# Performance work log

Hardware: AMD Instinct MI355X
Metric: run time of the kernel (lower is better)

Reference implementation:

```python
import jax, jax.numpy as jnp
import numpy as np

B, C, T, NB, NF = 4, 256, 128, 64, 512

def _rms(x, w, eps=1e-6):
    # RMSNorm over channel dim (axis=1) of NCHW tensor
    return x * jax.lax.rsqrt(jnp.mean(x * x, axis=1, keepdims=True) + eps) * w[None, :, None, None]

def _conv1(x, w, b):
    # 1x1 conv: w is [out, in]
    return jnp.einsum('bchw,oc->bohw', x, w) + b[None, :, None, None]

def _swiglu(x, iw, ib, ow, ob):
    h = _conv1(x, iw, ib)
    a, g = jnp.split(h, 2, axis=1)
    return _conv1(a * jax.nn.silu(g), ow, ob)

def setup_inputs() -> dict:
    key = jax.random.key(0)
    ks = iter(jax.random.split(key, 32))
    s = lambda shape, scale: jax.random.normal(next(ks), shape, jnp.float32) * scale
    wsc = 1.0 / np.sqrt(C)
    return {
        'latent': s((B, C, T, NB), 1.0),
        'side': s((B, C, T, NF), 1.0),
        'expansion_basis': s((1, NB, 1, NF), 1.0),
        'lp_norm_w': jnp.ones((C,), jnp.float32),
        'lp_w': s((C, C), wsc), 'lp_b': jnp.zeros((C,), jnp.float32),
        'qn_w': jnp.ones((C,), jnp.float32),
        'qmlp_in_w': s((2 * C, C), wsc), 'qmlp_in_b': jnp.zeros((2 * C,), jnp.float32),
        'qmlp_out_w': s((C, C), wsc), 'qmlp_out_b': jnp.zeros((C,), jnp.float32),
        'q_w': s((C, C), wsc), 'q_b': jnp.zeros((C,), jnp.float32),
        'k_w': s((C, C), wsc), 'k_b': jnp.zeros((C,), jnp.float32),
        'v_w': s((C, C), wsc), 'v_b': jnp.zeros((C,), jnp.float32),
        'o_w': s((C, C), wsc), 'o_b': jnp.zeros((C,), jnp.float32),
        'ffn_norm_w': jnp.ones((C,), jnp.float32),
        'ffn_in_w': s((2 * C, C), wsc), 'ffn_in_b': jnp.zeros((2 * C,), jnp.float32),
        'ffn_out_w': s((C, C), wsc), 'ffn_out_b': jnp.zeros((C,), jnp.float32),
        'score_scale': jnp.asarray(1.0 / np.sqrt(C), jnp.float32),
        'prior_scale': jnp.asarray(1.0, jnp.float32),
        'query_skip_scale': jnp.asarray(1.0, jnp.float32),
    }

def reference(latent, side, expansion_basis, lp_norm_w, lp_w, lp_b, qn_w,
              qmlp_in_w, qmlp_in_b, qmlp_out_w, qmlp_out_b,
              q_w, q_b, k_w, k_b, v_w, v_b, o_w, o_b,
              ffn_norm_w, ffn_in_w, ffn_in_b, ffn_out_w, ffn_out_b,
              score_scale, prior_scale, query_skip_scale):
    # latent_pre: RMSNorm -> 1x1 conv -> SiLU
    latent_h = jax.nn.silu(_conv1(_rms(latent, lp_norm_w), lp_w, lp_b))  # [B,C,T,NB]
    # adaptive query path
    query_h = _swiglu(_rms(side, qn_w), qmlp_in_w, qmlp_in_b, qmlp_out_w, qmlp_out_b)  # [B,C,T,NF]
    q = _conv1(query_h, q_w, q_b)   # [B,C,T,NF]
    k = _conv1(latent_h, k_w, k_b)  # [B,C,T,NB]
    v = _conv1(latent_h, v_w, v_b)  # [B,C,T,NB]
    # scores: [B,T,NF,NB], contraction over channel
    scores = jnp.einsum('bctf,bctn->btfn', q, k) * score_scale
    bias = expansion_basis[0, :, 0, :].T  # [NF, NB]
    scores = scores + bias[None, None] * prior_scale
    weights = jax.nn.softmax(scores, axis=-1)
    attended = jnp.einsum('btfn,bctn->bctf', weights, v)  # [B,C,T,NF]
    hidden = _conv1(attended, o_w, o_b) + query_h * query_skip_scale
    hidden = hidden + _swiglu(_rms(hidden, ffn_norm_w), ffn_in_w, ffn_in_b, ffn_out_w, ffn_out_b)
    return hidden
```

## Files before the change

kernel.cpp:

```cpp
#include <hip/hip_runtime.h>
#include <stdint.h>
#include <stddef.h>

#define B_ 4
#define C_ 256
#define T_ 128
#define NB_ 64
#define NF_ 512
#define PLAT_ (T_*NB_)
#define PSIDE_ (T_*NF_)

using bf16x8 = __attribute__((ext_vector_type(8))) short;
using bf16x4 = __attribute__((ext_vector_type(4))) short;
using f32x4  = __attribute__((ext_vector_type(4))) float;

__device__ __forceinline__ float b2f(unsigned short h) {
  unsigned int u = ((unsigned int)h) << 16;
  return __builtin_bit_cast(float, u);
}
__device__ __forceinline__ unsigned short f2b(float f) {
  unsigned int u = __builtin_bit_cast(unsigned int, f);
  u += 0x7FFFu + ((u >> 16) & 1u);
  return (unsigned short)(u >> 16);
}

__device__ __forceinline__ bf16x8 ld8(const unsigned short* p) {
  return *(const bf16x8*)p;
}
__device__ __forceinline__ bf16x8 ld8(const float* p) {
  float4 a = *(const float4*)p;
  float4 b = *(const float4*)(p + 4);
  bf16x8 r;
  r[0] = (short)f2b(a.x); r[1] = (short)f2b(a.y);
  r[2] = (short)f2b(a.z); r[3] = (short)f2b(a.w);
  r[4] = (short)f2b(b.x); r[5] = (short)f2b(b.y);
  r[6] = (short)f2b(b.z); r[7] = (short)f2b(b.w);
  return r;
}
__device__ __forceinline__ float ldv(float v) { return v; }
__device__ __forceinline__ float ldv(unsigned short v) { return b2f(v); }
__device__ __forceinline__ void stv(float* p, float v) { *p = v; }
__device__ __forceinline__ void stv(unsigned short* p, float v) { *p = f2b(v); }

__device__ __forceinline__ void gload16(const void* g, void* l) {
  __builtin_amdgcn_global_load_lds(
      (const __attribute__((address_space(1))) void*)g,
      (__attribute__((address_space(3))) void*)l, 16, 0, 0);
}

__device__ __forceinline__ int u4i(int r) { return (r ^ (r >> 2)) & 3; }

enum { EPI_NONE = 0, EPI_SILU = 1, EPI_RESID = 3, EPI_SWIGLU = 4, EPI_DUALX = 5 };

__global__ __launch_bounds__(256) void wprep_k(const float* __restrict__ w,
                                               const float* __restrict__ nw,
                                               unsigned short* __restrict__ out, int n)
{
  int i = blockIdx.x * 256 + threadIdx.x;
  if (i < n) out[i] = f2b(w[i] * nw[i & 255]);
}

__global__ __launch_bounds__(256) void cvt_k(const float* __restrict__ in,
                                             unsigned short* __restrict__ out, int n)
{
  int i = blockIdx.x * 256 + threadIdx.x;
  if (i < n) out[i] = f2b(in[i]);
}

__global__ __launch_bounds__(256) void wscale_k(const float* __restrict__ w,
                                                const float* __restrict__ s,
                                                unsigned short* __restrict__ out, int n)
{
  int i = blockIdx.x * 256 + threadIdx.x;
  if (i < n) out[i] = f2b(w[i] * s[0]);
}

__global__ __launch_bounds__(256) void foldw_k(const float* __restrict__ A,
                                               const float* __restrict__ Bm,
                                               unsigned short* __restrict__ out)
{
  const int m = blockIdx.x;
  const int c = threadIdx.x;
  float acc = 0.f;
  #pragma unroll 8
  for (int j = 0; j < C_; ++j) acc = fmaf(A[m * C_ + j], Bm[j * C_ + c], acc);
  out[m * C_ + c] = f2b(acc);
}

__global__ __launch_bounds__(256) void foldb_k(const float* __restrict__ A,
                                               const float* __restrict__ bin,
                                               const float* __restrict__ badd,
                                               float* __restrict__ bout)
{
  const int m = threadIdx.x;
  float acc = 0.f;
  #pragma unroll 8
  for (int j = 0; j < C_; ++j) acc = fmaf(A[m * C_ + j], bin[j], acc);
  bout[m] = acc + badd[m];
}

__global__ __launch_bounds__(256) void bcomb_k(const float* __restrict__ b0,
                                               const float* __restrict__ b1,
                                               const float* __restrict__ s,
                                               float* __restrict__ bout)
{
  const int m = threadIdx.x;
  bout[m] = b0[m] + s[0] * b1[m];
}

template<int EPI, bool RMS, bool XT, typename TY, bool YT, int CFG>
__global__ __launch_bounds__(256, 2) void gemm_k(
    const void* __restrict__ Xv,
    const void* __restrict__ Xv2,
    const unsigned short* __restrict__ W,
    const float* __restrict__ bias,
    TY* Y,
    unsigned short* Y2,
    int Xs, int Xoff, int Ys, int Yoff, int Ys2)
{
  constexpr bool WDUAL = (EPI == EPI_SWIGLU) || (EPI == EPI_DUALX);
  constexpr bool GDUAL = (EPI == EPI_SWIGLU);
  constexpr bool XDUAL = (EPI == EPI_DUALX);
  constexpr bool H2    = (EPI == EPI_DUALX);
  constexpr int NWV = (CFG == 0) ? 1 : 2;
  constexpr int BM  = (CFG == 0) ? 256 : 128;
  constexpr int WN  = 64 / NWV;
  constexpr int NFR = WN / 16;
  constexpr int RW  = (WDUAL ? 2 : 1) * BM;
  constexpr int XR  = (XDUAL ? 2 : 1) * 64;

  __shared__ unsigned short sA[RW * 32];
  __shared__ unsigned short sX[XR * 32];
  __shared__ float red[4][64];

  const int tid = threadIdx.x;
  const int lane = tid & 63;
  const int wid = tid >> 6;
  const int l15 = lane & 15;
  const int q4 = lane >> 4;
  const int z = blockIdx.z;
  const int p0 = blockIdx.x * 64;
  const int m0 = blockIdx.y * BM;
  const int mh = (CFG == 0) ? wid : (wid >> 1);
  const int nh = (CFG == 0) ? 0 : (wid & 1);

  const float* Xf = nullptr;
  const unsigned short* Xt = nullptr;
  const unsigned short* Xt2 = nullptr;
  if constexpr (XT) {
    Xt = (const unsigned short*)Xv + ((size_t)z * Xs + Xoff + p0) * C_;
    if constexpr (XDUAL)
      Xt2 = (const unsigned short*)Xv2 + ((size_t)z * Xs + Xoff + p0) * C_;
  } else {
    Xf = (const float*)Xv + (size_t)z * C_ * Xs + Xoff + p0;
  }

  const f32x4 zf = {0.f, 0.f, 0.f, 0.f};
  f32x4 acc0[4][NFR];
  f32x4 acc1[GDUAL ? 4 : 1][NFR];
  #pragma unroll
  for (int i = 0; i < 4; ++i)
    #pragma unroll
    for (int j = 0; j < NFR; ++j) {
      acc0[i][j] = zf;
      if constexpr (GDUAL) acc1[i][j] = zf;
    }

  float sq = 0.f;

  for (int kt = 0; kt < 8; ++kt) {
    if constexpr (XT) {
      const int row = wid * 16 + (lane >> 2);
      const int chunk = (lane & 3) ^ u4i(row);
      const size_t soff = (size_t)row * C_ + kt * 32 + (chunk << 3);
      gload16(Xt + soff, &sX[(wid * 16) * 32]);
      if constexpr (XDUAL) gload16(Xt2 + soff, &sX[(64 + wid * 16) * 32]);
    } else {
      const float* xp = Xf + (size_t)(kt * 32 + wid * 8) * Xs + lane;
      float v[8];
      #pragma unroll
      for (int j = 0; j < 8; ++j) v[j] = xp[(size_t)j * Xs];
      bf16x8 w8;
      #pragma unroll
      for (int j = 0; j < 8; ++j) {
        if constexpr (RMS) sq = fmaf(v[j], v[j], sq);
        w8[j] = (short)f2b(v[j]);
      }
      *(bf16x8*)((char*)sX + lane * 64 + ((wid ^ u4i(lane)) << 4)) = w8;
    }
    #pragma unroll
    for (int it = 0; it < RW / 64; ++it) {
      const int rbase = wid * (RW / 4) + it * 16;
      const int rl = rbase + (lane >> 2);
      const int bank = rl / BM;
      const int rloc = rl & (BM - 1);
      const int chunk = (lane & 3) ^ u4i(rl);
      gload16(W + (size_t)(bank * C_ + m0 + rloc) * C_ + kt * 32 + (chunk << 3),
              &sA[rbase * 32]);
    }
    __syncthreads();

    bf16x8 af0[4], af1[4], bfr[NFR], bfr2[NFR];
    #pragma unroll
    for (int mf = 0; mf < 4; ++mf) {
      const int r = mh * 64 + mf * 16 + l15;
      const int sl = (q4 ^ u4i(r)) << 3;
      af0[mf] = *(const bf16x8*)(&sA[r * 32 + sl]);
      if constexpr (WDUAL) af1[mf] = *(const bf16x8*)(&sA[(BM + r) * 32 + sl]);
    }
    #pragma unroll
    for (int nf = 0; nf < NFR; ++nf) {
      const int n = nh * WN + nf * 16 + l15;
      const int sl = (q4 ^ u4i(n)) << 3;
      bfr[nf] = *(const bf16x8*)(&sX[n * 32 + sl]);
      if constexpr (XDUAL) bfr2[nf] = *(const bf16x8*)(&sX[(64 + n) * 32 + sl]);
    }
    #pragma unroll
    for (int mf = 0; mf < 4; ++mf)
      #pragma unroll
      for (int nf = 0; nf < NFR; ++nf) {
        acc0[mf][nf] = __builtin_amdgcn_mfma_f32_16x16x32_bf16(af0[mf], bfr[nf], acc0[mf][nf], 0, 0, 0);
        if constexpr (GDUAL)
          acc1[mf][nf] = __builtin_amdgcn_mfma_f32_16x16x32_bf16(af1[mf], bfr[nf], acc1[mf][nf], 0, 0, 0);
        if constexpr (XDUAL)
          acc0[mf][nf] = __builtin_amdgcn_mfma_f32_16x16x32_bf16(af1[mf], bfr2[nf], acc0[mf][nf], 0, 0, 0);
      }
    __syncthreads();
  }

  float cs[NFR];
  #pragma unroll
  for (int nf = 0; nf < NFR; ++nf) cs[nf] = 1.f;
  if constexpr (RMS) {
    red[wid][lane] = sq;
    __syncthreads();
    #pragma unroll
    for (int nf = 0; nf < NFR; ++nf) {
      const int n = nh * WN + nf * 16 + l15;
      cs[nf] = rsqrtf((red[0][n] + red[1][n] + red[2][n] + red[3][n]) * (1.0f / (float)C_) + 1e-6f);
    }
  }

  TY* Yb = nullptr;
  if constexpr (!YT) Yb = Y + (size_t)z * C_ * Ys + Yoff;

  float p2[NFR];
  #pragma unroll
  for (int nf = 0; nf < NFR; ++nf) p2[nf] = 0.f;

  #pragma unroll
  for (int mf = 0; mf < 4; ++mf) {
    const int mb = m0 + mh * 64 + mf * 16 + q4 * 4;
    const float4 b1 = *(const float4*)(bias + mb);
    float4 b2 = {0.f, 0.f, 0.f, 0.f};
    if constexpr (GDUAL) b2 = *(const float4*)(bias + C_ + mb);
    #pragma unroll
    for (int nf = 0; nf < NFR; ++nf) {
      const int pl = p0 + nh * WN + nf * 16 + l15;
      if constexpr (YT) {
        bf16x4 pk;
        #pragma unroll
        for (int r = 0; r < 4; ++r) {
          float y = acc0[mf][nf][r] * cs[nf] + ((const float*)&b1)[r];
          if constexpr (EPI == EPI_SILU) y = y / (1.0f + __expf(-y));
          if constexpr (EPI == EPI_SWIGLU) {
            float g = acc1[mf][nf][r] * cs[nf] + ((const float*)&b2)[r];
            y = y * (g / (1.0f + __expf(-g)));
          }
          pk[r] = (short)f2b(y);
        }
        *(bf16x4*)(Y + ((size_t)z * Ys + Yoff + pl) * C_ + mb) = pk;
      } else {
        #pragma unroll
        for (int r = 0; r < 4; ++r) {
          const size_t oidx = (size_t)(mb + r) * Ys + pl;
          float y = acc0[mf][nf][r] * cs[nf] + ((const float*)&b1)[r];
          if constexpr (EPI == EPI_SILU) y = y / (1.0f + __expf(-y));
          if constexpr (EPI == EPI_SWIGLU) {
            float g = acc1[mf][nf][r] * cs[nf] + ((const float*)&b2)[r];
            y = y * (g / (1.0f + __expf(-g)));
          }
          if constexpr (EPI == EPI_RESID) y += ldv(Yb[oidx]);
          if constexpr (H2) p2[nf] = fmaf(y, y, p2[nf]);
          stv(&Yb[oidx], y);
        }
      }
    }
  }

  if constexpr (H2) {
    #pragma unroll
    for (int nf = 0; nf < NFR; ++nf) {
      p2[nf] += __shfl_xor(p2[nf], 16);
      p2[nf] += __shfl_xor(p2[nf], 32);
    }
    if (q4 == 0) {
      #pragma unroll
      for (int nf = 0; nf < NFR; ++nf) red[wid][nf * 16 + l15] = p2[nf];
    }
    __syncthreads();
    float cs2[NFR];
    #pragma unroll
    for (int nf = 0; nf < NFR; ++nf) {
      const int n = nf * 16 + l15;
      cs2[nf] = rsqrtf((red[0][n] + red[1][n] + red[2][n] + red[3][n]) * (1.0f / (float)C_) + 1e-6f);
    }
    #pragma unroll
    for (int mf = 0; mf < 4; ++mf) {
      const int mb = m0 + mh * 64 + mf * 16 + q4 * 4;
      const float4 b1 = *(const float4*)(bias + mb);
      #pragma unroll
      for (int nf = 0; nf < NFR; ++nf) {
        const int pl = p0 + nf * 16 + l15;
        bf16x4 pk;
        #pragma unroll
        for (int r = 0; r < 4; ++r) {
          const float h = (acc0[mf][nf][r] + ((const float*)&b1)[r]) * cs2[nf];
          pk[r] = (short)f2b(h);
        }
        *(bf16x4*)(Y2 + ((size_t)z * Ys2 + pl) * C_ + mb) = pk;
      }
    }
  }
}

__global__ __launch_bounds__(256) void attn_k(
    const unsigned short* Q,
    const unsigned short* __restrict__ Kp,
    const unsigned short* __restrict__ Vp,
    const float* __restrict__ basis,
    const float* __restrict__ ssp,
    const float* __restrict__ psp,
    unsigned short* O,
    int PsQ, int t0, int ltc)
{
  __shared__ unsigned short sK[64 * 256];
  __shared__ unsigned short sQ[64 * 256];
  __shared__ unsigned short sV[256 * 72];
  __shared__ unsigned short sW[64 * 72];
  __shared__ unsigned short sB[64 * 72];

  const int tid = threadIdx.x;
  const int lane = tid & 63;
  const int wid = tid >> 6;
  const int l15 = lane & 15;
  const int q4 = lane >> 4;
  const int z = blockIdx.x >> ltc;
  const int tl = blockIdx.x & ((1 << ltc) - 1);

  const unsigned short* Qt = Q + ((size_t)z * PsQ + (size_t)tl * NF_) * C_;
  unsigned short*       Ot = O + ((size_t)z * PsQ + (size_t)tl * NF_) * C_;
  const unsigned short* Kt = Kp + ((size_t)z * PLAT_ + (size_t)(t0 + tl) * NB_) * C_;
  const size_t vbase = (size_t)z * C_ * PLAT_ + (size_t)(t0 + tl) * NB_;

  const float ss = ssp[0];
  const float ps = psp[0];
  const f32x4 zf = {0.f, 0.f, 0.f, 0.f};

  {
    #pragma unroll
    for (int it = 0; it < 8; ++it) {
      int i = wid * 8 + it;
      int n = 2 * i + (lane >> 5);
      int sc = (lane & 31) ^ (n & 7);
      gload16(Kt + (size_t)n * C_ + (sc << 3), &sK[i * 512]);
    }
    const int c0 = tid >> 3;
    const int n0 = (tid & 7) << 3;
    #pragma unroll
    for (int pass = 0; pass < 8; ++pass) {
      int c = c0 + pass * 32;
      bf16x8 v8 = *(const bf16x8*)(Vp + vbase + (size_t)c * PLAT_ + n0);
      *(bf16x8*)(&sV[c * 72 + n0]) = v8;
    }
  }

  for (int fc = 0; fc < 8; ++fc) {
    const int f0 = fc * 64;
    #pragma unroll
    for (int it = 0; it < 8; ++it) {
      int i = wid * 8 + it;
      int n = 2 * i + (lane >> 5);
      int sc = (lane & 31) ^ (n & 7);
      gload16(Qt + (size_t)(f0 + n) * C_ + (sc << 3), &sQ[i * 512]);
    }
    {
      const int nr = tid >> 3;
      const int fl0 = (tid & 7) << 3;
      #pragma unroll
      for (int pass = 0; pass < 2; ++pass) {
        int nn = nr + pass * 32;
        bf16x8 b8 = ld8(basis + (size_t)nn * NF_ + f0 + fl0);
        *(bf16x8*)(&sB[nn * 72 + fl0]) = b8;
      }
    }
    __syncthreads();

    f32x4 sacc[4];
    #pragma unroll
    for (int nt = 0; nt < 4; ++nt) sacc[nt] = zf;
    const int frow = wid * 16 + l15;
    const int swq = l15 & 7;
    #pragma unroll
    for (int kt = 0; kt < 8; ++kt) {
      int kb = kt * 4 + q4;
      bf16x8 a8 = *(const bf16x8*)(&sQ[frow * 256 + ((kb ^ swq) << 3)]);
      #pragma unroll
      for (int nt = 0; nt < 4; ++nt) {
        bf16x8 b8 = *(const bf16x8*)(&sK[(nt * 16 + l15) * 256 + ((kb ^ swq) << 3)]);
        sacc[nt] = __builtin_amdgcn_mfma_f32_16x16x32_bf16(a8, b8, sacc[nt], 0, 0, 0);
      }
    }

    #pragma unroll
    for (int r = 0; r < 4; ++r) {
      const int fcl = wid * 16 + q4 * 4 + r;
      float v[4];
      #pragma unroll
      for (int nt = 0; nt < 4; ++nt)
        v[nt] = sacc[nt][r] * ss + b2f(sB[(nt * 16 + l15) * 72 + fcl]) * ps;
      float mx = fmaxf(fmaxf(v[0], v[1]), fmaxf(v[2], v[3]));
      #pragma unroll
      for (int d = 1; d < 16; d <<= 1) mx = fmaxf(mx, __shfl_xor(mx, d));
      float e[4], sum = 0.f;
      #pragma unroll
      for (int nt = 0; nt < 4; ++nt) { e[nt] = __expf(v[nt] - mx); sum += e[nt]; }
      #pragma unroll
      for (int d = 1; d < 16; d <<= 1) sum += __shfl_xor(sum, d);
      float inv = 1.0f / sum;
      #pragma unroll
      for (int nt = 0; nt < 4; ++nt)
        sW[fcl * 72 + nt * 16 + l15] = f2b(e[nt] * inv);
    }
    __syncthreads();

    f32x4 pacc[4][4];
    #pragma unroll
    for (int mf = 0; mf < 4; ++mf)
      #pragma unroll
      for (int nf = 0; nf < 4; ++nf) pacc[mf][nf] = zf;
    #pragma unroll
    for (int kt = 0; kt < 2; ++kt) {
      int k0 = kt * 32 + q4 * 8;
      bf16x8 a8[4], b8[4];
      #pragma unroll
      for (int mf = 0; mf < 4; ++mf)
        a8[mf] = *(const bf16x8*)(&sV[(wid * 64 + mf * 16 + l15) * 72 + k0]);
      #pragma unroll
      for (int nf = 0; nf < 4; ++nf)
        b8[nf] = *(const bf16x8*)(&sW[(nf * 16 + l15) * 72 + k0]);
      #pragma unroll
      for (int mf = 0; mf < 4; ++mf)
        #pragma unroll
        for (int nf = 0; nf < 4; ++nf)
          pacc[mf][nf] = __builtin_amdgcn_mfma_f32_16x16x32_bf16(a8[mf], b8[nf], pacc[mf][nf], 0, 0, 0);
    }
    #pragma unroll
    for (int mf = 0; mf < 4; ++mf) {
      int cb = wid * 64 + mf * 16 + q4 * 4;
      #pragma unroll
      for (int nf = 0; nf < 4; ++nf) {
        int f = f0 + nf * 16 + l15;
        bf16x4 pk;
        #pragma unroll
        for (int r = 0; r < 4; ++r) pk[r] = (short)f2b(pacc[mf][nf][r]);
        *(bf16x4*)(Ot + (size_t)f * C_ + cb) = pk;
      }
    }
    __syncthreads();
  }
}

extern "C" void kernel_launch(void* const* d_in, const int* in_sizes, int n_in,
                              void* d_out, int out_size, void* d_ws, size_t ws_size,
                              hipStream_t stream)
{
  (void)in_sizes; (void)n_in; (void)out_size;
  const float* latent     = (const float*)d_in[0];
  const float* side       = (const float*)d_in[1];
  const float* basis      = (const float*)d_in[2];
  const float* lp_norm_w  = (const float*)d_in[3];
  const float* lp_w       = (const float*)d_in[4];
  const float* lp_b       = (const float*)d_in[5];
  const float* qn_w       = (const float*)d_in[6];
  const float* qmlp_in_w  = (const float*)d_in[7];
  const float* qmlp_in_b  = (const float*)d_in[8];
  const float* qmlp_out_w = (const float*)d_in[9];
  const float* qmlp_out_b = (const float*)d_in[10];
  const float* q_w        = (const float*)d_in[11];
  const float* q_b        = (const float*)d_in[12];
  const float* k_w        = (const float*)d_in[13];
  const float* k_b        = (const float*)d_in[14];
  const float* v_w        = (const float*)d_in[15];
  const float* v_b        = (const float*)d_in[16];
  const float* o_w        = (const float*)d_in[17];
  const float* o_b        = (const float*)d_in[18];
  const float* ffn_norm_w = (const float*)d_in[19];
  const float* ffn_in_w   = (const float*)d_in[20];
  const float* ffn_in_b   = (const float*)d_in[21];
  const float* ffn_out_w  = (const float*)d_in[22];
  const float* ffn_out_b  = (const float*)d_in[23];
  const float* sc_scale   = (const float*)d_in[24];
  const float* pr_scale   = (const float*)d_in[25];
  const float* qk_scale   = (const float*)d_in[26];
  float* out = (float*)d_out;

  auto align256 = [](size_t b) { return (b + 255) & ~(size_t)255; };
  const size_t fixed_bytes =
      5 * align256((size_t)C_ * C_ * 2) +
      3 * align256((size_t)2 * C_ * C_ * 2) +
      2 * align256((size_t)C_ * 4) +
      3 * align256((size_t)B_ * C_ * PLAT_ * 2);
  int nc = 16;
  for (int c = 1; c <= 16; c <<= 1) {
    size_t Pcb = (size_t)PSIDE_ / c;
    size_t need = fixed_bytes + 2 * align256((size_t)B_ * C_ * Pcb * 2);
    if (need <= ws_size) { nc = c; break; }
  }
  const int Pc  = PSIDE_ / nc;
  const int Tc  = T_ / nc;
  int ltc = 0; while ((1 << ltc) < Tc) ++ltc;

  char* ws = (char*)d_ws;
  size_t off = 0;
  auto carve = [&](size_t bytes) -> char* {
    char* p = ws + off;
    off += (bytes + 255) & ~(size_t)255;
    return p;
  };
  unsigned short* wlp      = (unsigned short*)carve((size_t)C_ * C_ * 2);
  unsigned short* wqin     = (unsigned short*)carve((size_t)2 * C_ * C_ * 2);
  unsigned short* wffin    = (unsigned short*)carve((size_t)2 * C_ * C_ * 2);
  unsigned short* wk       = (unsigned short*)carve((size_t)C_ * C_ * 2);
  unsigned short* wv       = (unsigned short*)carve((size_t)C_ * C_ * 2);
  unsigned short* wfo      = (unsigned short*)carve((size_t)C_ * C_ * 2);
  unsigned short* wqeff    = (unsigned short*)carve((size_t)C_ * C_ * 2);
  unsigned short* wocat    = (unsigned short*)carve((size_t)2 * C_ * C_ * 2);
  float*          beff     = (float*)carve((size_t)C_ * 4);
  float*          bcomb    = (float*)carve((size_t)C_ * 4);
  unsigned short* latent_h = (unsigned short*)carve((size_t)B_ * C_ * PLAT_ * 2);
  unsigned short* kbuf     = (unsigned short*)carve((size_t)B_ * C_ * PLAT_ * 2);
  unsigned short* vbuf     = (unsigned short*)carve((size_t)B_ * C_ * PLAT_ * 2);
  unsigned short* big0     = (unsigned short*)carve((size_t)B_ * C_ * Pc * 2);
  unsigned short* qbuf     = (unsigned short*)carve((size_t)B_ * C_ * Pc * 2);

  const dim3 blk(256);
  const dim3 gLatA(PLAT_ / 64, 1, B_);
  const dim3 gChA(Pc / 64, 1, B_);
  const dim3 gChB(Pc / 64, 2, B_);
  const int NW = C_ * C_;

  wprep_k<<<dim3(NW / 256), blk, 0, stream>>>(lp_w, lp_norm_w, wlp, NW);
  wprep_k<<<dim3(2 * NW / 256), blk, 0, stream>>>(qmlp_in_w, qn_w, wqin, 2 * NW);
  wprep_k<<<dim3(2 * NW / 256), blk, 0, stream>>>(ffn_in_w, ffn_norm_w, wffin, 2 * NW);
  cvt_k<<<dim3(NW / 256), blk, 0, stream>>>(k_w, wk, NW);
  cvt_k<<<dim3(NW / 256), blk, 0, stream>>>(v_w, wv, NW);
  cvt_k<<<dim3(NW / 256), blk, 0, stream>>>(ffn_out_w, wfo, NW);
  foldw_k<<<dim3(C_), blk, 0, stream>>>(q_w, qmlp_out_w, wqeff);
  foldb_k<<<dim3(1), blk, 0, stream>>>(q_w, qmlp_out_b, q_b, beff);
  cvt_k<<<dim3(NW / 256), blk, 0, stream>>>(o_w, wocat, NW);
  wscale_k<<<dim3(NW / 256), blk, 0, stream>>>(qmlp_out_w, qk_scale, wocat + (size_t)NW, NW);
  bcomb_k<<<dim3(1), blk, 0, stream>>>(o_b, qmlp_out_b, qk_scale, bcomb);

  gemm_k<EPI_SILU, true, false, unsigned short, true, 0><<<gLatA, blk, 0, stream>>>(
      latent, nullptr, wlp, lp_b, latent_h, nullptr, PLAT_, 0, PLAT_, 0, 0);
  gemm_k<EPI_NONE, false, true, unsigned short, true, 0><<<gLatA, blk, 0, stream>>>(
      latent_h, nullptr, wk, k_b, kbuf, nullptr, PLAT_, 0, PLAT_, 0, 0);
  gemm_k<EPI_NONE, false, true, unsigned short, false, 0><<<gLatA, blk, 0, stream>>>(
      latent_h, nullptr, wv, v_b, vbuf, nullptr, PLAT_, 0, PLAT_, 0, 0);

  for (int ch = 0; ch < nc; ++ch) {
    const int co = ch * Pc;
    const int t0 = ch * Tc;
    gemm_k<EPI_SWIGLU, true, false, unsigned short, true, 1><<<gChB, blk, 0, stream>>>(
        side, nullptr, wqin, qmlp_in_b, big0, nullptr, PSIDE_, co, Pc, 0, 0);
    gemm_k<EPI_NONE, false, true, unsigned short, true, 0><<<gChA, blk, 0, stream>>>(
        big0, nullptr, wqeff, beff, qbuf, nullptr, Pc, 0, Pc, 0, 0);
    attn_k<<<dim3(B_ * Tc), blk, 0, stream>>>(qbuf, kbuf, vbuf, basis, sc_scale, pr_scale,
                                              qbuf, Pc, t0, ltc);
    gemm_k<EPI_DUALX, false, true, float, false, 0><<<gChA, blk, 0, stream>>>(
        qbuf, big0, wocat, bcomb, out, qbuf, Pc, 0, PSIDE_, co, Pc);
    gemm_k<EPI_SWIGLU, false, true, unsigned short, true, 1><<<gChB, blk, 0, stream>>>(
        qbuf, nullptr, wffin, ffn_in_b, big0, nullptr, Pc, 0, Pc, 0, 0);
    gemm_k<EPI_RESID, false, true, float, false, 0><<<gChA, blk, 0, stream>>>(
        big0, nullptr, wfo, ffn_out_b, out, nullptr, Pc, 0, PSIDE_, co, 0);
  }
}
```

Baseline: 1.457 ms.

## Defer FFN RMS scaling to consumer GEMM and keep hidden in bf16

The DUALX GEMM no longer writes fp32 hidden to the output plus a normalized bf16 copy. It now writes unnormalized bf16 hidden into qbuf along with a per-position RMS scale vector. The FFN-in GEMM applies that scale in its epilogue (CSIN), and the final residual GEMM reads the bf16 hidden from qbuf instead of reading back fp32 output. This removes an fp32 write and read of the full output plus a second accumulator pass, at the cost of holding the residual in bf16 precision. The CFG1 grid is also flattened so the two M-halves of a pixel tile are adjacent block indices.

```diff
diff --git a/kernel.cpp b/kernel.cpp
--- a/kernel.cpp
+++ b/kernel.cpp
@@ -16,6 +16,10 @@
 
 __device__ __forceinline__ float b2f(unsigned short h) {
   unsigned int u = ((unsigned int)h) << 16;
+  return __builtin_bit_cast(float, u);
+}
+__device__ __forceinline__ float b2f(short h) {
+  unsigned int u = ((unsigned int)(unsigned short)h) << 16;
   return __builtin_bit_cast(float, u);
 }
 __device__ __forceinline__ unsigned short f2b(float f) {
@@ -37,8 +41,6 @@
   r[6] = (short)f2b(b.z); r[7] = (short)f2b(b.w);
   return r;
 }
-__device__ __forceinline__ float ldv(float v) { return v; }
-__device__ __forceinline__ float ldv(unsigned short v) { return b2f(v); }
 __device__ __forceinline__ void stv(float* p, float v) { *p = v; }
 __device__ __forceinline__ void stv(unsigned short* p, float v) { *p = f2b(v); }
 
@@ -108,22 +110,22 @@
   bout[m] = b0[m] + s[0] * b1[m];
 }
 
-template<int EPI, bool RMS, bool XT, typename TY, bool YT, int CFG>
+template<int EPI, bool RMS, bool XT, typename TY, bool YT, int CFG, bool CSIN>
 __global__ __launch_bounds__(256, 2) void gemm_k(
     const void* __restrict__ Xv,
     const void* __restrict__ Xv2,
     const unsigned short* __restrict__ W,
     const float* __restrict__ bias,
     TY* Y,
-    unsigned short* Y2,
-    int Xs, int Xoff, int Ys, int Yoff, int Ys2)
+    const unsigned short* __restrict__ RT,
+    float* pscale,
+    int Xs, int Xoff, int Ys, int Yoff, int Ps)
 {
   constexpr bool WDUAL = (EPI == EPI_SWIGLU) || (EPI == EPI_DUALX);
   constexpr bool GDUAL = (EPI == EPI_SWIGLU);
   constexpr bool XDUAL = (EPI == EPI_DUALX);
-  constexpr bool H2    = (EPI == EPI_DUALX);
+  constexpr int BM  = (CFG == 0) ? 256 : 128;
   constexpr int NWV = (CFG == 0) ? 1 : 2;
-  constexpr int BM  = (CFG == 0) ? 256 : 128;
   constexpr int WN  = 64 / NWV;
   constexpr int NFR = WN / 16;
   constexpr int RW  = (WDUAL ? 2 : 1) * BM;
@@ -139,8 +141,8 @@
   const int l15 = lane & 15;
   const int q4 = lane >> 4;
   const int z = blockIdx.z;
-  const int p0 = blockIdx.x * 64;
-  const int m0 = blockIdx.y * BM;
+  const int p0 = ((CFG == 0) ? blockIdx.x : (blockIdx.x >> 1)) * 64;
+  const int m0 = (CFG == 0) ? 0 : (blockIdx.x & 1) * BM;
   const int mh = (CFG == 0) ? wid : (wid >> 1);
   const int nh = (CFG == 0) ? 0 : (wid & 1);
 
@@ -240,6 +242,11 @@
       cs[nf] = rsqrtf((red[0][n] + red[1][n] + red[2][n] + red[3][n]) * (1.0f / (float)C_) + 1e-6f);
     }
   }
+  if constexpr (CSIN) {
+    #pragma unroll
+    for (int nf = 0; nf < NFR; ++nf)
+      cs[nf] = pscale[(size_t)z * Ps + p0 + nh * WN + nf * 16 + l15];
+  }
 
   TY* Yb = nullptr;
   if constexpr (!YT) Yb = Y + (size_t)z * C_ * Ys + Yoff;
@@ -257,6 +264,9 @@
     #pragma unroll
     for (int nf = 0; nf < NFR; ++nf) {
       const int pl = p0 + nh * WN + nf * 16 + l15;
+      bf16x4 h4 = {0, 0, 0, 0};
+      if constexpr (EPI == EPI_RESID)
+        h4 = *(const bf16x4*)(RT + ((size_t)z * Ps + pl) * C_ + mb);
       if constexpr (YT) {
         bf16x4 pk;
         #pragma unroll
@@ -267,6 +277,7 @@
             float g = acc1[mf][nf][r] * cs[nf] + ((const float*)&b2)[r];
             y = y * (g / (1.0f + __expf(-g)));
           }
+          if constexpr (EPI == EPI_DUALX) p2[nf] = fmaf(y, y, p2[nf]);
           pk[r] = (short)f2b(y);
         }
         *(bf16x4*)(Y + ((size_t)z * Ys + Yoff + pl) * C_ + mb) = pk;
@@ -280,15 +291,14 @@
             float g = acc1[mf][nf][r] * cs[nf] + ((const float*)&b2)[r];
             y = y * (g / (1.0f + __expf(-g)));
           }
-          if constexpr (EPI == EPI_RESID) y += ldv(Yb[oidx]);
-          if constexpr (H2) p2[nf] = fmaf(y, y, p2[nf]);
+          if constexpr (EPI == EPI_RESID) y += b2f(h4[r]);
           stv(&Yb[oidx], y);
         }
       }
     }
   }
 
-  if constexpr (H2) {
+  if constexpr (EPI == EPI_DUALX) {
     #pragma unroll
     for (int nf = 0; nf < NFR; ++nf) {
       p2[nf] += __shfl_xor(p2[nf], 16);
@@ -299,26 +309,12 @@
       for (int nf = 0; nf < NFR; ++nf) red[wid][nf * 16 + l15] = p2[nf];
     }
     __syncthreads();
-    float cs2[NFR];
-    #pragma unroll
-    for (int nf = 0; nf < NFR; ++nf) {
-      const int n = nf * 16 + l15;
-      cs2[nf] = rsqrtf((red[0][n] + red[1][n] + red[2][n] + red[3][n]) * (1.0f / (float)C_) + 1e-6f);
-    }
-    #pragma unroll
-    for (int mf = 0; mf < 4; ++mf) {
-      const int mb = m0 + mh * 64 + mf * 16 + q4 * 4;
-      const float4 b1 = *(const float4*)(bias + mb);
+    if (wid == 0 && q4 == 0) {
       #pragma unroll
       for (int nf = 0; nf < NFR; ++nf) {
-        const int pl = p0 + nf * 16 + l15;
-        bf16x4 pk;
-        #pragma unroll
-        for (int r = 0; r < 4; ++r) {
-          const float h = (acc0[mf][nf][r] + ((const float*)&b1)[r]) * cs2[nf];
-          pk[r] = (short)f2b(h);
-        }
-        *(bf16x4*)(Y2 + ((size_t)z * Ys2 + pl) * C_ + mb) = pk;
+        const int n = nf * 16 + l15;
+        const float c2 = rsqrtf((red[0][n] + red[1][n] + red[2][n] + red[3][n]) * (1.0f / (float)C_) + 1e-6f);
+        pscale[(size_t)z * Ps + p0 + n] = c2;
       }
     }
   }
@@ -514,7 +510,8 @@
   int nc = 16;
   for (int c = 1; c <= 16; c <<= 1) {
     size_t Pcb = (size_t)PSIDE_ / c;
-    size_t need = fixed_bytes + 2 * align256((size_t)B_ * C_ * Pcb * 2);
+    size_t need = fixed_bytes + 2 * align256((size_t)B_ * C_ * Pcb * 2)
+                + align256((size_t)B_ * Pcb * 4);
     if (need <= ws_size) { nc = c; break; }
   }
   const int Pc  = PSIDE_ / nc;
@@ -543,11 +540,12 @@
   unsigned short* vbuf     = (unsigned short*)carve((size_t)B_ * C_ * PLAT_ * 2);
   unsigned short* big0     = (unsigned short*)carve((size_t)B_ * C_ * Pc * 2);
   unsigned short* qbuf     = (unsigned short*)carve((size_t)B_ * C_ * Pc * 2);
+  float*          pscale   = (float*)carve((size_t)B_ * Pc * 4);
 
   const dim3 blk(256);
   const dim3 gLatA(PLAT_ / 64, 1, B_);
   const dim3 gChA(Pc / 64, 1, B_);
-  const dim3 gChB(Pc / 64, 2, B_);
+  const dim3 gChB(Pc / 64 * 2, 1, B_);
   const int NW = C_ * C_;
 
   wprep_k<<<dim3(NW / 256), blk, 0, stream>>>(lp_w, lp_norm_w, wlp, NW);
@@ -562,27 +560,27 @@
   wscale_k<<<dim3(NW / 256), blk, 0, stream>>>(qmlp_out_w, qk_scale, wocat + (size_t)NW, NW);
   bcomb_k<<<dim3(1), blk, 0, stream>>>(o_b, qmlp_out_b, qk_scale, bcomb);
 
-  gemm_k<EPI_SILU, true, false, unsigned short, true, 0><<<gLatA, blk, 0, stream>>>(
-      latent, nullptr, wlp, lp_b, latent_h, nullptr, PLAT_, 0, PLAT_, 0, 0);
-  gemm_k<EPI_NONE, false, true, unsigned short, true, 0><<<gLatA, blk, 0, stream>>>(
-      latent_h, nullptr, wk, k_b, kbuf, nullptr, PLAT_, 0, PLAT_, 0, 0);
-  gemm_k<EPI_NONE, false, true, unsigned short, false, 0><<<gLatA, blk, 0, stream>>>(
-      latent_h, nullptr, wv, v_b, vbuf, nullptr, PLAT_, 0, PLAT_, 0, 0);
+  gemm_k<EPI_SILU, true, false, unsigned short, true, 0, false><<<gLatA, blk, 0, stream>>>(
+      latent, nullptr, wlp, lp_b, latent_h, nullptr, nullptr, PLAT_, 0, PLAT_, 0, 0);
+  gemm_k<EPI_NONE, false, true, unsigned short, true, 0, false><<<gLatA, blk, 0, stream>>>(
+      latent_h, nullptr, wk, k_b, kbuf, nullptr, nullptr, PLAT_, 0, PLAT_, 0, 0);
+  gemm_k<EPI_NONE, false, true, unsigned short, false, 0, false><<<gLatA, blk, 0, stream>>>(
+      latent_h, nullptr, wv, v_b, vbuf, nullptr, nullptr, PLAT_, 0, PLAT_, 0, 0);
 
   for (int ch = 0; ch < nc; ++ch) {
     const int co = ch * Pc;
     const int t0 = ch * Tc;
-    gemm_k<EPI_SWIGLU, true, false, unsigned short, true, 1><<<gChB, blk, 0, stream>>>(
-        side, nullptr, wqin, qmlp_in_b, big0, nullptr, PSIDE_, co, Pc, 0, 0);
-    gemm_k<EPI_NONE, false, true, unsigned short, true, 0><<<gChA, blk, 0, stream>>>(
-        big0, nullptr, wqeff, beff, qbuf, nullptr, Pc, 0, Pc, 0, 0);
+    gemm_k<EPI_SWIGLU, true, false, unsigned short, true, 1, false><<<gChB, blk, 0, stream>>>(
+        side, nullptr, wqin, qmlp_in_b, big0, nullptr, nullptr, PSIDE_, co, Pc, 0, 0);
+    gemm_k<EPI_NONE, false, true, unsigned short, true, 0, false><<<gChA, blk, 0, stream>>>(
+        big0, nullptr, wqeff, beff, qbuf, nullptr, nullptr, Pc, 0, Pc, 0, 0);
     attn_k<<<dim3(B_ * Tc), blk, 0, stream>>>(qbuf, kbuf, vbuf, basis, sc_scale, pr_scale,
                                               qbuf, Pc, t0, ltc);
-    gemm_k<EPI_DUALX, false, true, float, false, 0><<<gChA, blk, 0, stream>>>(
-        qbuf, big0, wocat, bcomb, out, qbuf, Pc, 0, PSIDE_, co, Pc);
-    gemm_k<EPI_SWIGLU, false, true, unsigned short, true, 1><<<gChB, blk, 0, stream>>>(
-        qbuf, nullptr, wffin, ffn_in_b, big0, nullptr, Pc, 0, Pc, 0, 0);
-    gemm_k<EPI_RESID, false, true, float, false, 0><<<gChA, blk, 0, stream>>>(
-        big0, nullptr, wfo, ffn_out_b, out, nullptr, Pc, 0, PSIDE_, co, 0);
-  }
-}
+    gemm_k<EPI_DUALX, false, true, unsigned short, true, 0, false><<<gChA, blk, 0, stream>>>(
+        qbuf, big0, wocat, bcomb, qbuf, nullptr, pscale, Pc, 0, Pc, 0, Pc);
+    gemm_k<EPI_SWIGLU, false, true, unsigned short, true, 1, true><<<gChB, blk, 0, stream>>>(
+        qbuf, nullptr, wffin, ffn_in_b, big0, nullptr, pscale, Pc, 0, Pc, 0, Pc);
+    gemm_k<EPI_RESID, false, true, float, false, 0, false><<<gChA, blk, 0, stream>>>(
+        big0, nullptr, wfo, ffn_out_b, out, qbuf, nullptr, Pc, 0, PSIDE_, co, Pc);
+  }
+}
```

New measurement: 1.285 ms. -11.8%, faster.
